# Kernel tuning notes

Hardware: AMD Instinct MI355X
Metric: run time of the kernel (lower is better)

The kernel has to match this reference:

```python
import jax, jax.numpy as jnp
import numpy as np

B, S, T = 2048, 32, 32
D, H = 128, 256       # cle_dim, rnn_dim
VS, VT = 256, 256     # source/target char vocab
BOW = 1               # MorphoDataset.Factor.BOW


def setup_inputs() -> dict:
    key = jax.random.key(0)
    ks = jax.random.split(key, 16)
    n = lambda k, sh: (jax.random.normal(k, sh, jnp.float32) * 0.05)
    inp = {
        "src_emb": n(ks[0], (VS, D)),
        "tgt_emb": n(ks[1], (VT, D)),
        "enc_f_W": n(ks[2], (D, 3 * H)),
        "enc_f_U": n(ks[3], (H, 3 * H)),
        "enc_f_b": jnp.zeros((2, 3 * H), jnp.float32),
        "enc_b_W": n(ks[4], (D, 3 * H)),
        "enc_b_U": n(ks[5], (H, 3 * H)),
        "enc_b_b": jnp.zeros((2, 3 * H), jnp.float32),
        "dec_W": n(ks[6], (D + H, 3 * H)),
        "dec_U": n(ks[7], (H, 3 * H)),
        "dec_b": jnp.zeros((2, 3 * H), jnp.float32),
        "out_W": n(ks[8], (H, VT)),
        "out_b": jnp.zeros((VT,), jnp.float32),
        "att_src_W": n(ks[9], (H, H)),
        "att_src_b": jnp.zeros((H,), jnp.float32),
        "att_st_W": n(ks[10], (H, H)),
        "att_st_b": jnp.zeros((H,), jnp.float32),
        "att_v": n(ks[11], (H, 1)),
        "att_v_b": jnp.zeros((1,), jnp.float32),
        "source_ids": jax.random.randint(ks[12], (B, S), 0, VS, jnp.int32),
        "target_ids": jax.random.randint(ks[13], (B, T), 0, VT, jnp.int32),
    }
    return inp


def _gru_step(h, x, W, U, b):
    # Keras GRU, reset_after=True: separate input/recurrent biases b[0], b[1]
    gx = x @ W + b[0]
    gh = h @ U + b[1]
    xz, xr, xh = jnp.split(gx, 3, axis=-1)
    hz, hr, hh = jnp.split(gh, 3, axis=-1)
    z = jax.nn.sigmoid(xz + hz)
    r = jax.nn.sigmoid(xr + hr)
    c = jnp.tanh(xh + r * hh)
    return z * h + (1.0 - z) * c


def _gru_scan(x_tbd, W, U, b):
    # x_tbd: [S, B, D] -> outputs [S, B, H]
    h0 = jnp.zeros((x_tbd.shape[1], U.shape[0]), x_tbd.dtype)
    def step(h, x):
        h = _gru_step(h, x, W, U, b)
        return h, h
    _, ys = jax.lax.scan(step, h0, x_tbd)
    return ys


def reference(src_emb, tgt_emb, enc_f_W, enc_f_U, enc_f_b, enc_b_W, enc_b_U, enc_b_b,
              dec_W, dec_U, dec_b, out_W, out_b, att_src_W, att_src_b,
              att_st_W, att_st_b, att_v, att_v_b, source_ids, target_ids):
    # ---- Encoder: bidirectional GRU, merge_mode='sum' ----
    x = src_emb[source_ids]                      # [B, S, D]
    x_t = jnp.transpose(x, (1, 0, 2))            # [S, B, D]
    fwd = _gru_scan(x_t, enc_f_W, enc_f_U, enc_f_b)
    bwd = _gru_scan(x_t[::-1], enc_b_W, enc_b_U, enc_b_b)[::-1]
    source_states = jnp.transpose(fwd + bwd, (1, 0, 2))  # [B, S, H]

    # projected source states are constant across decoder steps -> precompute
    proj_src = source_states @ att_src_W + att_src_b     # [B, S, H]

    def attend(inp, h):
        p = h @ att_st_W + att_st_b                      # [B, H]
        e = jnp.tanh(proj_src + p[:, None, :]) @ att_v + att_v_b  # [B, S, 1]
        w = jax.nn.softmax(e, axis=1)                    # softmax over source positions
        ctx = jnp.sum(source_states * w, axis=1)         # [B, H]
        return jnp.concatenate([inp, ctx], axis=1)       # [B, D+H]

    # ---- Decoder (teacher forcing) ----
    h0 = source_states[:, 0]                             # [B, H]
    bow = jnp.broadcast_to(tgt_emb[BOW], (source_ids.shape[0], tgt_emb.shape[1]))
    inp0 = attend(bow, h0)

    def dstep(carry, tgt_t):
        h, inp = carry
        h = _gru_step(h, inp, dec_W, dec_U, dec_b)       # GRUCell step
        logits = h @ out_W + out_b                       # [B, VT]
        nxt = attend(tgt_emb[tgt_t], h)
        return (h, nxt), logits

    _, logits = jax.lax.scan(dstep, (h0, inp0), jnp.transpose(target_ids))
    return jnp.transpose(logits, (1, 0, 2))              # [B, T, VT]
```

## Files before the change

kernel.cpp:

```cpp
#include <hip/hip_runtime.h>
#include <math.h>

#define B_  2048
#define S_  32
#define T_  32
#define D_  128
#define H_  256
#define G3  768
#define VT_ 256
#define BOW_ 1

typedef __attribute__((ext_vector_type(8))) short short8;
typedef __attribute__((ext_vector_type(4))) float f32x4;
typedef __attribute__((ext_vector_type(8))) unsigned short us8;
typedef unsigned short u16;

__device__ inline u16 f2bf(float x) {
  union { float f; unsigned u; } v; v.f = x;
  unsigned r = v.u + 0x7FFFu + ((v.u >> 16) & 1u);
  return (u16)(r >> 16);
}
__device__ inline float bf2f(u16 b) {
  union { unsigned u; float f; } v; v.u = ((unsigned)b) << 16; return v.f;
}
__device__ inline int swz(int r) { return ((r ^ (r >> 3)) & 7) << 3; }
__device__ inline float sigm(float x) { return 1.f / (1.f + expf(-x)); }

struct TMat { const float* src; u16* dhi; u16* dlo; int R; int C; int tile0; };
struct TPack { TMat m[10]; };

__global__ __launch_bounds__(256)
void wsplit_t(TPack P) {
  int bx = blockIdx.x;
  TMat M = P.m[0];
  #pragma unroll
  for (int i = 1; i < 10; i++) if (bx >= P.m[i].tile0) M = P.m[i];
  int ti = bx - M.tile0;
  int tilesR = M.R >> 6;
  int rt = ti % tilesR, ct = ti / tilesR;
  int r0 = rt * 64, c0 = ct * 64;
  __shared__ float ts[64][65];
  int tid = threadIdx.x;
  int cx = tid & 63, ry = tid >> 6;
  #pragma unroll
  for (int i = 0; i < 16; i++) {
    int r = ry * 16 + i;
    ts[r][cx] = M.src[(size_t)(r0 + r) * M.C + c0 + cx];
  }
  __syncthreads();
  int rx = tid & 63, cy = tid >> 6;
  #pragma unroll
  for (int i = 0; i < 16; i++) {
    int cc = cy * 16 + i;
    float v = ts[rx][cc];
    u16 hi = f2bf(v);
    size_t o = (size_t)(c0 + cc) * M.R + r0 + rx;
    M.dhi[o] = hi;
    M.dlo[o] = f2bf(v - bf2f(hi));
  }
}

__global__ __launch_bounds__(256)
void esplit(const float* a, const float* b, u16* ah, u16* al, u16* bh, u16* bl, int n) {
  int i = blockIdx.x * 256 + threadIdx.x;
  if (i >= 2 * n) return;
  const float* s = (i < n) ? a : b;
  u16* dh = (i < n) ? ah : bh;
  u16* dl = (i < n) ? al : bl;
  int j = (i < n) ? i : i - n;
  float v = s[j];
  u16 hi = f2bf(v);
  dh[j] = hi; dl[j] = f2bf(v - bf2f(hi));
}

struct PLeg {
  const u16* Ahi; const u16* Alo; int lda;
  const u16* Bthi; const u16* Btlo; int ldb;
  const float* bias; void* C; int ldc; int cmode;
  int M, N, K;
};

__global__ __launch_bounds__(256)
void gemm_pl(PLeg l0, PLeg l1) {
  PLeg L = blockIdx.z ? l1 : l0;
  int n0 = blockIdx.x * 128; if (n0 >= L.N) return;
  int m0 = blockIdx.y * 128; if (m0 >= L.M) return;
  __shared__ u16 As[128 * 64];
  __shared__ u16 Bs[128 * 64];
  int tid = threadIdx.x;
  int lane = tid & 63, wv = tid >> 6;
  int wr = (wv >> 1) * 64, wc = (wv & 1) * 64;
  int fr = lane & 15, fk = (lane >> 4) * 8;
  f32x4 acc[4][4];
  #pragma unroll
  for (int m = 0; m < 4; m++)
    #pragma unroll
    for (int n = 0; n < 4; n++) acc[m][n] = (f32x4){0.f, 0.f, 0.f, 0.f};

  int s_row = tid >> 1, s_part = tid & 1;

  for (int k0 = 0; k0 < L.K; k0 += 32) {
    if (k0) __syncthreads();
    int swA = swz(s_row);
    {
      const u16* src = (s_part ? L.Alo : L.Ahi) + (size_t)(m0 + s_row) * L.lda + k0;
      #pragma unroll
      for (int q = 0; q < 4; q++)
        *(us8*)&As[(s_row * 64 + s_part * 32 + q * 8) ^ swA] = *(const us8*)(src + q * 8);
    }
    {
      const u16* src = (s_part ? L.Btlo : L.Bthi) + (size_t)(n0 + s_row) * L.ldb + k0;
      #pragma unroll
      for (int q = 0; q < 4; q++)
        *(us8*)&Bs[(s_row * 64 + s_part * 32 + q * 8) ^ swA] = *(const us8*)(src + q * 8);
    }
    __syncthreads();
    short8 bhi[4], blo[4];
    #pragma unroll
    for (int n = 0; n < 4; n++) {
      int cc = wc + n * 16 + fr; int sw = swz(cc);
      bhi[n] = *(const short8*)&Bs[(cc * 64 + fk) ^ sw];
      blo[n] = *(const short8*)&Bs[(cc * 64 + 32 + fk) ^ sw];
    }
    #pragma unroll
    for (int m = 0; m < 4; m++) {
      int r = wr + m * 16 + fr; int sw = swz(r);
      short8 ahi = *(const short8*)&As[(r * 64 + fk) ^ sw];
      short8 alo = *(const short8*)&As[(r * 64 + 32 + fk) ^ sw];
      #pragma unroll
      for (int n = 0; n < 4; n++) {
        acc[m][n] = __builtin_amdgcn_mfma_f32_16x16x32_bf16(ahi, bhi[n], acc[m][n], 0, 0, 0);
        acc[m][n] = __builtin_amdgcn_mfma_f32_16x16x32_bf16(ahi, blo[n], acc[m][n], 0, 0, 0);
        acc[m][n] = __builtin_amdgcn_mfma_f32_16x16x32_bf16(alo, bhi[n], acc[m][n], 0, 0, 0);
      }
    }
  }
  int rbase = (lane >> 4) * 4;
  #pragma unroll
  for (int m = 0; m < 4; m++)
    #pragma unroll
    for (int rr = 0; rr < 4; rr++) {
      int row = m0 + wr + m * 16 + rbase + rr;
      #pragma unroll
      for (int n = 0; n < 4; n++) {
        int col = n0 + wc + n * 16 + fr;
        float v = acc[m][n][rr];
        if (L.bias) v += L.bias[col];
        if (L.cmode == 0)      ((float*)L.C)[(size_t)row * L.ldc + col] = v;
        else if (L.cmode == 1) ((u16*)L.C)[(size_t)row * L.ldc + col] = f2bf(v);
        else {
          size_t o = (((size_t)(row & (B_ - 1))) * T_ + (row >> 11)) * VT_ + col;
          ((float*)L.C)[o] = v;
        }
      }
    }
}

struct GruDesc {
  const u16 *a0H, *a0L;
  const u16 *a1H, *a1L;
  const u16 *b0H, *b0L;
  const u16 *b1H, *b1L;
  const float *gxT;
  const float *bias0, *bias1;
  const float *hold;
  const u16 *holdH, *holdL;
  float *hnew;
  u16 *hh, *hl;
  u16 *ssH, *ssL;
  const int *ids;
  int ssmode;
  int sidx, rev;
};

template<int MODE>
__global__ __launch_bounds__(256)
void gru_step(GruDesc d0, GruDesc d1) {
  GruDesc D = blockIdx.z ? d1 : d0;
  constexpr int KT  = MODE ? 512 : 256;
  constexpr int KT8 = KT / 8;
  constexpr int MF  = MODE ? 1 : 2;
  constexpr int NST = KT / 32;
  __shared__ __align__(16) u16 As[2 * 32 * KT];

  int m0 = blockIdx.y * 32;
  int tid = threadIdx.x;
  int lane = tid & 63, wv = tid >> 6;
  int fr = lane & 15, kq = lane >> 4;
  int jn, rb0;
  if (MODE == 0) { jn = blockIdx.x * 64 + wv * 16 + fr; rb0 = 0; }
  else           { jn = blockIdx.x * 32 + (wv & 1) * 16 + fr; rb0 = (wv >> 1) * 16; }

  constexpr int PER_T = (2 * 32 * KT8) / 256;
  #pragma unroll
  for (int i = 0; i < PER_T; i++) {
    int s = tid + i * 256;
    int p = s / (32 * KT8);
    int rem = s - p * (32 * KT8);
    int row = rem / KT8;
    int kb = rem - row * KT8;
    int k = kb * 8;
    const u16* src;
    if (MODE == 0) {
      src = (p ? D.a0L : D.a0H) + (size_t)(m0 + row) * 256 + k;
    } else {
      src = (k < 256) ? (p ? D.a0L : D.a0H) + (size_t)(m0 + row) * 256 + k
                      : (p ? D.a1L : D.a1H) + (size_t)(m0 + row) * 256 + (k - 256);
    }
    *(us8*)&As[(s ^ (row & 7)) * 8] = *(const us8*)src;
  }
  __syncthreads();

  f32x4 acc[4][MF];
  #pragma unroll
  for (int a = 0; a < 4; a++)
    #pragma unroll
    for (int mf = 0; mf < MF; mf++) acc[a][mf] = (f32x4){0.f, 0.f, 0.f, 0.f};

  #pragma unroll
  for (int i = 0; i < NST; i++) {
    const u16 *BH, *BL; int bk, ai2;
    if (MODE == 0)    { BH = D.b0H; BL = D.b0L; bk = i * 32; ai2 = 2; }
    else if (i < 8)   { BH = D.b0H; BL = D.b0L; bk = i * 32; ai2 = 2; }
    else              { BH = D.b1H; BL = D.b1L; bk = (i - 8) * 32; ai2 = 3; }
    short8 ah[MF], al[MF];
    #pragma unroll
    for (int mf = 0; mf < MF; mf++) {
      int rp = rb0 + mf * 16 + fr;
      int kb = i * 4 + kq;
      ah[mf] = *(const short8*)&As[((rp * KT8 + kb) ^ (fr & 7)) * 8];
      al[mf] = *(const short8*)&As[((32 * KT8 + rp * KT8 + kb) ^ (fr & 7)) * 8];
    }
    #pragma unroll
    for (int st = 0; st < 3; st++) {
      size_t ro = (size_t)(st * 256 + jn) * 256 + bk + kq * 8;
      short8 bh = *(const short8*)(BH + ro);
      short8 bl = *(const short8*)(BL + ro);
      int ai = (st < 2) ? st : ai2;
      #pragma unroll
      for (int mf = 0; mf < MF; mf++) {
        acc[ai][mf] = __builtin_amdgcn_mfma_f32_16x16x32_bf16(ah[mf], bh, acc[ai][mf], 0, 0, 0);
        acc[ai][mf] = __builtin_amdgcn_mfma_f32_16x16x32_bf16(ah[mf], bl, acc[ai][mf], 0, 0, 0);
        acc[ai][mf] = __builtin_amdgcn_mfma_f32_16x16x32_bf16(al[mf], bh, acc[ai][mf], 0, 0, 0);
      }
    }
  }

  int rbase = kq * 4;
  int j = jn;
  float b0z = D.bias0[j],       b1z = D.bias1[j];
  float b0r = D.bias0[256 + j], b1r = D.bias1[256 + j];
  float b0c = D.bias0[512 + j], b1c = D.bias1[512 + j];
  #pragma unroll
  for (int mf = 0; mf < MF; mf++)
    #pragma unroll
    for (int rr = 0; rr < 4; rr++) {
      int b = m0 + rb0 + mf * 16 + rbase + rr;
      size_t o = (size_t)b * H_ + j;
      int id;
      if (MODE == 0) id = D.ids[b * S_ + (D.rev ? (S_ - 1 - D.sidx) : D.sidx)];
      else           id = (D.sidx == 0) ? BOW_ : D.ids[b * T_ + D.sidx - 1];
      const float* T = D.gxT + (size_t)id * G3;
      float z = sigm(acc[0][mf][rr] + T[j] + b0z + b1z);
      float r = sigm(acc[1][mf][rr] + T[256 + j] + b0r + b1r);
      float xc = T[512 + j] + b0c + (MODE ? acc[3][mf][rr] : 0.f);
      float c = tanhf(xc + r * (acc[2][mf][rr] + b1c));
      float hprev = D.hold ? D.hold[o] : (bf2f(D.holdH[o]) + bf2f(D.holdL[o]));
      float hn = z * hprev + (1.f - z) * c;
      D.hnew[o] = hn;
      u16 hi = f2bf(hn);
      D.hh[o] = hi; D.hl[o] = f2bf(hn - bf2f(hi));
      if (MODE == 0) {
        if (D.ssmode == 1) {
          D.ssH[o] = hi; D.ssL[o] = f2bf(hn - bf2f(hi));
        } else if (D.ssmode == 2) {
          float v = bf2f(D.ssH[o]) + bf2f(D.ssL[o]) + hn;
          u16 vh = f2bf(v);
          D.ssH[o] = vh; D.ssL[o] = f2bf(v - bf2f(vh));
        }
      }
    }
}

__global__ __launch_bounds__(256)
void attend_k(const u16* __restrict__ projbf, const u16* __restrict__ ssH,
              const float* __restrict__ p, const float* __restrict__ att_v,
              u16* __restrict__ ctxh, u16* __restrict__ ctxl) {
  int b = blockIdx.x;
  int tid = threadIdx.x;
  int lane = tid & 63;
  int wv = tid >> 6;
  __shared__ float e_s[S_];
  __shared__ float w_s[S_];
  float pq[4], vq[4];
  #pragma unroll
  for (int q = 0; q < 4; q++) {
    pq[q] = p[(size_t)b * H_ + q * 64 + lane];
    vq[q] = att_v[q * 64 + lane];
  }
  float pv[8][4];
  #pragma unroll
  for (int i = 0; i < 8; i++) {
    const u16* pr = projbf + ((size_t)(wv * 8 + i) * B_ + b) * H_;
    #pragma unroll
    for (int q = 0; q < 4; q++) pv[i][q] = bf2f(pr[q * 64 + lane]);
  }
  u16 sv[S_];
  #pragma unroll
  for (int s = 0; s < S_; s++) sv[s] = ssH[((size_t)s * B_ + b) * H_ + tid];

  #pragma unroll
  for (int i = 0; i < 8; i++) {
    float part = 0.f;
    #pragma unroll
    for (int q = 0; q < 4; q++)
      part += tanhf(pv[i][q] + pq[q]) * vq[q];
    #pragma unroll
    for (int off = 32; off; off >>= 1)
      part += __shfl_xor(part, off);
    if (lane == 0) e_s[wv * 8 + i] = part;
  }
  __syncthreads();
  float m = -1e30f;
  #pragma unroll
  for (int s = 0; s < S_; s++) m = fmaxf(m, e_s[s]);
  float den = 0.f;
  #pragma unroll
  for (int s = 0; s < S_; s++) den += expf(e_s[s] - m);
  if (tid < S_) w_s[tid] = expf(e_s[tid] - m) / den;
  __syncthreads();
  float acc = 0.f;
  #pragma unroll
  for (int s = 0; s < S_; s++)
    acc = fmaf(w_s[s], bf2f(sv[s]), acc);
  u16 hi = f2bf(acc);
  size_t o = (size_t)b * H_ + tid;
  ctxh[o] = hi; ctxl[o] = f2bf(acc - bf2f(hi));
}

extern "C" void kernel_launch(void* const* d_in, const int* in_sizes, int n_in,
                              void* d_out, int out_size, void* d_ws, size_t ws_size,
                              hipStream_t stream) {
  const float* src_emb   = (const float*)d_in[0];
  const float* tgt_emb   = (const float*)d_in[1];
  const float* enc_f_W   = (const float*)d_in[2];
  const float* enc_f_U   = (const float*)d_in[3];
  const float* enc_f_b   = (const float*)d_in[4];
  const float* enc_b_W   = (const float*)d_in[5];
  const float* enc_b_U   = (const float*)d_in[6];
  const float* enc_b_b   = (const float*)d_in[7];
  const float* dec_W     = (const float*)d_in[8];
  const float* dec_U     = (const float*)d_in[9];
  const float* dec_b     = (const float*)d_in[10];
  const float* out_W     = (const float*)d_in[11];
  const float* out_b     = (const float*)d_in[12];
  const float* att_src_W = (const float*)d_in[13];
  const float* att_src_b = (const float*)d_in[14];
  const float* att_st_W  = (const float*)d_in[15];
  const float* att_st_b  = (const float*)d_in[16];
  const float* att_v     = (const float*)d_in[17];
  const int* source_ids  = (const int*)d_in[19];
  const int* target_ids  = (const int*)d_in[20];
  float* out = (float*)d_out;

  char* base = (char*)d_ws;
  size_t off = 0;
  auto allocB = [&](size_t bytes) { void* p = base + off; off = (off + bytes + 255) & ~255UL; return p; };
  const size_t BH = (size_t)B_ * H_;

  u16* ssH    = (u16*)allocB((size_t)S_ * BH * 2);
  u16* ssL    = (u16*)allocB((size_t)S_ * BH * 2);
  u16* projbf = (u16*)allocB((size_t)S_ * BH * 2);
  float* pbuf = (float*)allocB(BH * 4);
  u16* ctxh = (u16*)allocB(BH * 2);
  u16* ctxl = (u16*)allocB(BH * 2);

  float* encF0 = (float*)allocB(2 * BH * 4);
  u16*  encPl0 = (u16*)allocB(4 * BH * 2);
  float* encF1 = (float*)allocB(2 * BH * 4);
  u16*  encPl1 = (u16*)allocB(4 * BH * 2);
  float* encF[2][2]  = { { encF0, encF0 + BH }, { encF1, encF1 + BH } };
  u16*  encH[2][2]   = { { encPl0, encPl0 + 2 * BH }, { encPl1, encPl1 + 2 * BH } };
  u16*  encL[2][2]   = { { encPl0 + BH, encPl0 + 3 * BH }, { encPl1 + BH, encPl1 + 3 * BH } };

  float* hDecF[2] = { (float*)allocB(BH * 4), (float*)allocB(BH * 4) };
  u16* hAllH = (u16*)allocB((size_t)T_ * BH * 2);
  u16* hAllL = (u16*)allocB((size_t)T_ * BH * 2);

  auto planes2 = [&](size_t n, u16*& h, u16*& l) { h = (u16*)allocB(n * 2); l = (u16*)allocB(n * 2); };
  u16 *UtFh,*UtFl,*UtBh,*UtBl,*WtFh,*WtFl,*WtBh,*WtBl;
  u16 *dUth,*dUtl,*dWcth,*dWctl,*dWxth,*dWxtl;
  u16 *oWth,*oWtl,*aStth,*aSttl,*aSrth,*aSrtl;
  u16 *sEh,*sEl,*tEh,*tEl;
  planes2((size_t)G3*H_, UtFh, UtFl);   planes2((size_t)G3*H_, UtBh, UtBl);
  planes2((size_t)G3*D_, WtFh, WtFl);   planes2((size_t)G3*D_, WtBh, WtBl);
  planes2((size_t)G3*H_, dUth, dUtl);   planes2((size_t)G3*H_, dWcth, dWctl);
  planes2((size_t)G3*D_, dWxth, dWxtl);
  planes2((size_t)H_*VT_, oWth, oWtl);
  planes2((size_t)H_*H_, aSrth, aSrtl);
  planes2((size_t)H_*H_, aStth, aSttl);
  planes2((size_t)VT_*D_, sEh, sEl);    planes2((size_t)VT_*D_, tEh, tEl);
  float* Tf = (float*)allocB((size_t)VT_ * G3 * 4);
  float* Tb = (float*)allocB((size_t)VT_ * G3 * 4);
  float* Td = (float*)allocB((size_t)VT_ * G3 * 4);

  TPack P;
  P.m[0] = { enc_f_U,          UtFh, UtFl, 256, 768, 0   };
  P.m[1] = { enc_b_U,          UtBh, UtBl, 256, 768, 48  };
  P.m[2] = { dec_U,            dUth, dUtl, 256, 768, 96  };
  P.m[3] = { dec_W + 128 * G3, dWcth, dWctl, 256, 768, 144 };
  P.m[4] = { enc_f_W,          WtFh, WtFl, 128, 768, 192 };
  P.m[5] = { enc_b_W,          WtBh, WtBl, 128, 768, 216 };
  P.m[6] = { dec_W,            dWxth, dWxtl, 128, 768, 240 };
  P.m[7] = { out_W,            oWth, oWtl, 256, 256, 264 };
  P.m[8] = { att_src_W,        aSrth, aSrtl, 256, 256, 280 };
  P.m[9] = { att_st_W,         aStth, aSttl, 256, 256, 296 };
  wsplit_t<<<312, 256, 0, stream>>>(P);
  esplit<<<(2 * VT_ * D_ + 255) / 256, 256, 0, stream>>>(src_emb, tgt_emb, sEh, sEl, tEh, tEl, VT_ * D_);

  {
    PLeg tf = { sEh, sEl, D_, WtFh, WtFl, D_, nullptr, Tf, G3, 0, VT_, G3, D_ };
    PLeg tb = { sEh, sEl, D_, WtBh, WtBl, D_, nullptr, Tb, G3, 0, VT_, G3, D_ };
    gemm_pl<<<dim3(6, 2, 2), 256, 0, stream>>>(tf, tb);
    PLeg td = { tEh, tEl, D_, dWxth, dWxtl, D_, nullptr, Td, G3, 0, VT_, G3, D_ };
    gemm_pl<<<dim3(6, 2, 1), 256, 0, stream>>>(td, td);
  }

  hipMemsetAsync(encF0, 0, 2 * BH * 4, stream);
  hipMemsetAsync(encPl0, 0, 4 * BH * 2, stream);

  for (int s = 0; s < S_; s++) {
    int p = s & 1;
    GruDesc dd[2];
    for (int d = 0; d < 2; d++) {
      GruDesc& D = dd[d];
      D.a0H = encH[p][d]; D.a0L = encL[p][d];
      D.a1H = nullptr; D.a1L = nullptr;
      D.b0H = d ? UtBh : UtFh; D.b0L = d ? UtBl : UtFl;
      D.b1H = nullptr; D.b1L = nullptr;
      D.gxT = d ? Tb : Tf;
      D.bias0 = d ? enc_b_b : enc_f_b;
      D.bias1 = (d ? enc_b_b : enc_f_b) + G3;
      D.hold = encF[p][d]; D.holdH = nullptr; D.holdL = nullptr;
      D.hnew = encF[p ^ 1][d];
      D.hh = encH[p ^ 1][d]; D.hl = encL[p ^ 1][d];
      int pos = d ? (S_ - 1 - s) : s;
      D.ssH = ssH + (size_t)pos * BH; D.ssL = ssL + (size_t)pos * BH;
      D.ids = source_ids;
      D.ssmode = (s < S_ / 2) ? 1 : 2;
      D.sidx = s; D.rev = d;
    }
    gru_step<0><<<dim3(4, 64, 2), 256, 0, stream>>>(dd[0], dd[1]);
  }

  {
    PLeg proj = { ssH, ssL, H_, aSrth, aSrtl, H_, att_src_b, projbf, H_, 1, S_ * B_, H_, H_ };
    PLeg p0   = { ssH, ssL, H_, aStth, aSttl, H_, att_st_b,  pbuf,   H_, 0, B_,      H_, H_ };
    gemm_pl<<<dim3(2, 512, 2), 256, 0, stream>>>(proj, p0);
  }
  attend_k<<<B_, 256, 0, stream>>>(projbf, ssH, pbuf, att_v, ctxh, ctxl);

  for (int t = 0; t < T_; t++) {
    int p = t & 1;
    GruDesc D = {};
    D.a0H = t ? hAllH + (size_t)(t - 1) * BH : ssH;
    D.a0L = t ? hAllL + (size_t)(t - 1) * BH : ssL;
    D.a1H = ctxh; D.a1L = ctxl;
    D.b0H = dUth;  D.b0L = dUtl;
    D.b1H = dWcth; D.b1L = dWctl;
    D.gxT = Td;
    D.bias0 = dec_b; D.bias1 = dec_b + G3;
    if (t == 0) { D.hold = nullptr; D.holdH = ssH; D.holdL = ssL; }
    else        { D.hold = hDecF[p]; D.holdH = nullptr; D.holdL = nullptr; }
    D.hnew = hDecF[p ^ 1];
    D.hh = hAllH + (size_t)t * BH; D.hl = hAllL + (size_t)t * BH;
    D.ssH = nullptr; D.ssL = nullptr;
    D.ids = target_ids;
    D.ssmode = 0; D.sidx = t; D.rev = 0;
    gru_step<1><<<dim3(8, 64, 1), 256, 0, stream>>>(D, D);

    if (t < T_ - 1) {
      PLeg LP = { hAllH + (size_t)t * BH, hAllL + (size_t)t * BH, H_,
                  aStth, aSttl, H_, att_st_b, pbuf, H_, 0, B_, H_, H_ };
      gemm_pl<<<dim3(2, 16, 1), 256, 0, stream>>>(LP, LP);
      attend_k<<<B_, 256, 0, stream>>>(projbf, ssH, pbuf, att_v, ctxh, ctxl);
    }
  }

  {
    PLeg LO = { hAllH, hAllL, H_, oWth, oWtl, H_, out_b, out, 0, 2, T_ * B_, VT_, H_ };
    gemm_pl<<<dim3(2, 512, 1), 256, 0, stream>>>(LO, LO);
  }
}
```

Baseline: 3.604 ms.

## Fuse encoder and decoder time loops into persistent cooperative kernels

Replaces the per-timestep encoder GRU launches and the per-step decoder GRU, projection-GEMM and attention launches with two persistent cooperative kernels that use grid-wide syncs between steps. The decoder attention phase fuses the query projection GEMM with the score, softmax and context computation in 128 blocks. The goal is to remove roughly 120 kernel launches and their launch gaps. In exchange it depends on cooperative-launch support and enough occupancy for 512 co-resident blocks, leaves most blocks idle during the attention phase, and falls back to per-step launches otherwise.

```diff
diff --git a/kernel.cpp b/kernel.cpp
--- a/kernel.cpp
+++ b/kernel.cpp
@@ -1,5 +1,8 @@
 #include <hip/hip_runtime.h>
+#include <hip/hip_cooperative_groups.h>
 #include <math.h>
+
+namespace cg = cooperative_groups;
 
 #define B_  2048
 #define S_  32
@@ -156,132 +159,6 @@
     }
 }
 
-struct GruDesc {
-  const u16 *a0H, *a0L;
-  const u16 *a1H, *a1L;
-  const u16 *b0H, *b0L;
-  const u16 *b1H, *b1L;
-  const float *gxT;
-  const float *bias0, *bias1;
-  const float *hold;
-  const u16 *holdH, *holdL;
-  float *hnew;
-  u16 *hh, *hl;
-  u16 *ssH, *ssL;
-  const int *ids;
-  int ssmode;
-  int sidx, rev;
-};
-
-template<int MODE>
-__global__ __launch_bounds__(256)
-void gru_step(GruDesc d0, GruDesc d1) {
-  GruDesc D = blockIdx.z ? d1 : d0;
-  constexpr int KT  = MODE ? 512 : 256;
-  constexpr int KT8 = KT / 8;
-  constexpr int MF  = MODE ? 1 : 2;
-  constexpr int NST = KT / 32;
-  __shared__ __align__(16) u16 As[2 * 32 * KT];
-
-  int m0 = blockIdx.y * 32;
-  int tid = threadIdx.x;
-  int lane = tid & 63, wv = tid >> 6;
-  int fr = lane & 15, kq = lane >> 4;
-  int jn, rb0;
-  if (MODE == 0) { jn = blockIdx.x * 64 + wv * 16 + fr; rb0 = 0; }
-  else           { jn = blockIdx.x * 32 + (wv & 1) * 16 + fr; rb0 = (wv >> 1) * 16; }
-
-  constexpr int PER_T = (2 * 32 * KT8) / 256;
-  #pragma unroll
-  for (int i = 0; i < PER_T; i++) {
-    int s = tid + i * 256;
-    int p = s / (32 * KT8);
-    int rem = s - p * (32 * KT8);
-    int row = rem / KT8;
-    int kb = rem - row * KT8;
-    int k = kb * 8;
-    const u16* src;
-    if (MODE == 0) {
-      src = (p ? D.a0L : D.a0H) + (size_t)(m0 + row) * 256 + k;
-    } else {
-      src = (k < 256) ? (p ? D.a0L : D.a0H) + (size_t)(m0 + row) * 256 + k
-                      : (p ? D.a1L : D.a1H) + (size_t)(m0 + row) * 256 + (k - 256);
-    }
-    *(us8*)&As[(s ^ (row & 7)) * 8] = *(const us8*)src;
-  }
-  __syncthreads();
-
-  f32x4 acc[4][MF];
-  #pragma unroll
-  for (int a = 0; a < 4; a++)
-    #pragma unroll
-    for (int mf = 0; mf < MF; mf++) acc[a][mf] = (f32x4){0.f, 0.f, 0.f, 0.f};
-
-  #pragma unroll
-  for (int i = 0; i < NST; i++) {
-    const u16 *BH, *BL; int bk, ai2;
-    if (MODE == 0)    { BH = D.b0H; BL = D.b0L; bk = i * 32; ai2 = 2; }
-    else if (i < 8)   { BH = D.b0H; BL = D.b0L; bk = i * 32; ai2 = 2; }
-    else              { BH = D.b1H; BL = D.b1L; bk = (i - 8) * 32; ai2 = 3; }
-    short8 ah[MF], al[MF];
-    #pragma unroll
-    for (int mf = 0; mf < MF; mf++) {
-      int rp = rb0 + mf * 16 + fr;
-      int kb = i * 4 + kq;
-      ah[mf] = *(const short8*)&As[((rp * KT8 + kb) ^ (fr & 7)) * 8];
-      al[mf] = *(const short8*)&As[((32 * KT8 + rp * KT8 + kb) ^ (fr & 7)) * 8];
-    }
-    #pragma unroll
-    for (int st = 0; st < 3; st++) {
-      size_t ro = (size_t)(st * 256 + jn) * 256 + bk + kq * 8;
-      short8 bh = *(const short8*)(BH + ro);
-      short8 bl = *(const short8*)(BL + ro);
-      int ai = (st < 2) ? st : ai2;
-      #pragma unroll
-      for (int mf = 0; mf < MF; mf++) {
-        acc[ai][mf] = __builtin_amdgcn_mfma_f32_16x16x32_bf16(ah[mf], bh, acc[ai][mf], 0, 0, 0);
-        acc[ai][mf] = __builtin_amdgcn_mfma_f32_16x16x32_bf16(ah[mf], bl, acc[ai][mf], 0, 0, 0);
-        acc[ai][mf] = __builtin_amdgcn_mfma_f32_16x16x32_bf16(al[mf], bh, acc[ai][mf], 0, 0, 0);
-      }
-    }
-  }
-
-  int rbase = kq * 4;
-  int j = jn;
-  float b0z = D.bias0[j],       b1z = D.bias1[j];
-  float b0r = D.bias0[256 + j], b1r = D.bias1[256 + j];
-  float b0c = D.bias0[512 + j], b1c = D.bias1[512 + j];
-  #pragma unroll
-  for (int mf = 0; mf < MF; mf++)
-    #pragma unroll
-    for (int rr = 0; rr < 4; rr++) {
-      int b = m0 + rb0 + mf * 16 + rbase + rr;
-      size_t o = (size_t)b * H_ + j;
-      int id;
-      if (MODE == 0) id = D.ids[b * S_ + (D.rev ? (S_ - 1 - D.sidx) : D.sidx)];
-      else           id = (D.sidx == 0) ? BOW_ : D.ids[b * T_ + D.sidx - 1];
-      const float* T = D.gxT + (size_t)id * G3;
-      float z = sigm(acc[0][mf][rr] + T[j] + b0z + b1z);
-      float r = sigm(acc[1][mf][rr] + T[256 + j] + b0r + b1r);
-      float xc = T[512 + j] + b0c + (MODE ? acc[3][mf][rr] : 0.f);
-      float c = tanhf(xc + r * (acc[2][mf][rr] + b1c));
-      float hprev = D.hold ? D.hold[o] : (bf2f(D.holdH[o]) + bf2f(D.holdL[o]));
-      float hn = z * hprev + (1.f - z) * c;
-      D.hnew[o] = hn;
-      u16 hi = f2bf(hn);
-      D.hh[o] = hi; D.hl[o] = f2bf(hn - bf2f(hi));
-      if (MODE == 0) {
-        if (D.ssmode == 1) {
-          D.ssH[o] = hi; D.ssL[o] = f2bf(hn - bf2f(hi));
-        } else if (D.ssmode == 2) {
-          float v = bf2f(D.ssH[o]) + bf2f(D.ssL[o]) + hn;
-          u16 vh = f2bf(v);
-          D.ssH[o] = vh; D.ssL[o] = f2bf(v - bf2f(vh));
-        }
-      }
-    }
-}
-
 __global__ __launch_bounds__(256)
 void attend_k(const u16* __restrict__ projbf, const u16* __restrict__ ssH,
               const float* __restrict__ p, const float* __restrict__ att_v,
@@ -336,6 +213,368 @@
   u16 hi = f2bf(acc);
   size_t o = (size_t)b * H_ + tid;
   ctxh[o] = hi; ctxl[o] = f2bf(acc - bf2f(hi));
+}
+
+struct EncP {
+  u16* hH[2][2]; u16* hL[2][2];
+  float* hF[2][2];
+  const u16 *bUH[2], *bUL[2];
+  const float *gxT[2];
+  const float *bias[2];
+  u16 *ssH, *ssL;
+  const int *ids;
+};
+
+__device__ __forceinline__ void enc_step_body(const EncP& P, int s, u16* As) {
+  int bid = blockIdx.x;
+  int d = bid >> 8, rem = bid & 255;
+  int x = rem & 3, y = rem >> 2;
+  int m0 = y * 32;
+  int tid = threadIdx.x;
+  int lane = tid & 63, wv = tid >> 6;
+  int fr = lane & 15, kq = lane >> 4;
+  int jn = x * 64 + wv * 16 + fr;
+  const size_t BHsz = (size_t)B_ * H_;
+
+  const u16 *bUH = P.bUH[d], *bUL = P.bUL[d];
+  const float *bias0 = P.bias[d], *bias1 = P.bias[d] + G3;
+  int par = s & 1;
+  const u16 *a0H = P.hH[par][d], *a0L = P.hL[par][d];
+
+  #pragma unroll
+  for (int i = 0; i < 8; i++) {
+    int sl = tid + i * 256;
+    int pl = sl >> 10;
+    int rm = sl & 1023;
+    int row = rm >> 5;
+    const u16* src = (pl ? a0L : a0H) + (size_t)(m0 + row) * 256 + (rm & 31) * 8;
+    *(us8*)&As[(sl ^ (row & 7)) * 8] = *(const us8*)src;
+  }
+  __syncthreads();
+
+  f32x4 acc[3][2];
+  #pragma unroll
+  for (int a = 0; a < 3; a++)
+    #pragma unroll
+    for (int mf = 0; mf < 2; mf++) acc[a][mf] = (f32x4){0.f, 0.f, 0.f, 0.f};
+
+  #pragma unroll
+  for (int i = 0; i < 8; i++) {
+    short8 ah[2], al[2];
+    #pragma unroll
+    for (int mf = 0; mf < 2; mf++) {
+      int rp = mf * 16 + fr;
+      int kb = i * 4 + kq;
+      ah[mf] = *(const short8*)&As[((rp * 32 + kb) ^ (fr & 7)) * 8];
+      al[mf] = *(const short8*)&As[((1024 + rp * 32 + kb) ^ (fr & 7)) * 8];
+    }
+    #pragma unroll
+    for (int st = 0; st < 3; st++) {
+      size_t ro = (size_t)(st * 256 + jn) * 256 + i * 32 + kq * 8;
+      short8 bh = *(const short8*)(bUH + ro);
+      short8 bl = *(const short8*)(bUL + ro);
+      #pragma unroll
+      for (int mf = 0; mf < 2; mf++) {
+        acc[st][mf] = __builtin_amdgcn_mfma_f32_16x16x32_bf16(ah[mf], bh, acc[st][mf], 0, 0, 0);
+        acc[st][mf] = __builtin_amdgcn_mfma_f32_16x16x32_bf16(ah[mf], bl, acc[st][mf], 0, 0, 0);
+        acc[st][mf] = __builtin_amdgcn_mfma_f32_16x16x32_bf16(al[mf], bh, acc[st][mf], 0, 0, 0);
+      }
+    }
+  }
+
+  float b0z = bias0[jn] + bias1[jn];
+  float b0r = bias0[256 + jn] + bias1[256 + jn];
+  float bxc = bias0[512 + jn];
+  float bhc = bias1[512 + jn];
+  const float *gxT = P.gxT[d];
+  int rbase = kq * 4;
+  float* hoF = P.hF[par][d];
+  float* hnF = P.hF[par ^ 1][d];
+  u16* hnH = P.hH[par ^ 1][d];
+  u16* hnL = P.hL[par ^ 1][d];
+  int pos = d ? (S_ - 1 - s) : s;
+  u16* ssHp = P.ssH + (size_t)pos * BHsz;
+  u16* ssLp = P.ssL + (size_t)pos * BHsz;
+  int ssmode = (s < S_ / 2) ? 1 : 2;
+  #pragma unroll
+  for (int mf = 0; mf < 2; mf++)
+    #pragma unroll
+    for (int rr = 0; rr < 4; rr++) {
+      int b = m0 + mf * 16 + rbase + rr;
+      size_t o = (size_t)b * H_ + jn;
+      int id = P.ids[b * S_ + (d ? (S_ - 1 - s) : s)];
+      const float* T = gxT + (size_t)id * G3;
+      float z = sigm(acc[0][mf][rr] + T[jn] + b0z);
+      float r = sigm(acc[1][mf][rr] + T[256 + jn] + b0r);
+      float c = tanhf(T[512 + jn] + bxc + r * (acc[2][mf][rr] + bhc));
+      float hn = z * hoF[o] + (1.f - z) * c;
+      hnF[o] = hn;
+      u16 hi = f2bf(hn);
+      u16 lo = f2bf(hn - bf2f(hi));
+      hnH[o] = hi; hnL[o] = lo;
+      if (ssmode == 1) {
+        ssHp[o] = hi; ssLp[o] = lo;
+      } else {
+        float v = bf2f(ssHp[o]) + bf2f(ssLp[o]) + hn;
+        u16 vh = f2bf(v);
+        ssHp[o] = vh; ssLp[o] = f2bf(v - bf2f(vh));
+      }
+    }
+}
+
+template<int COOP>
+__global__ __launch_bounds__(256, 2)
+void enc_all(EncP P, int s_single) {
+  __shared__ __align__(16) u16 As[2 * 32 * 256];
+  if constexpr (COOP) {
+    cg::grid_group grid = cg::this_grid();
+    for (int s = 0; s < S_; s++) {
+      enc_step_body(P, s, As);
+      if (s < S_ - 1) grid.sync();
+    }
+  } else {
+    enc_step_body(P, s_single, As);
+  }
+}
+
+struct DecP {
+  u16 *hAH, *hAL;
+  const u16 *s0H, *s0L;
+  float *hF[2];
+  u16 *ctxH, *ctxL;
+  const u16 *bUH, *bUL, *bCH, *bCL;
+  const float *gxT;
+  const float *bias;
+  const u16 *sWH, *sWL;
+  const float *stb;
+  const u16 *projbf, *ssHall;
+  const float *attv;
+  const int *ids;
+};
+
+__device__ __forceinline__ void dec_g_body(const DecP& P, int t, u16* As) {
+  int bid = blockIdx.x;
+  int tid = threadIdx.x;
+  int lane = tid & 63, wv = tid >> 6;
+  int fr = lane & 15, kq = lane >> 4;
+  int xg = bid & 7, yg = bid >> 3;
+  int m0 = yg * 32;
+  int jn = xg * 32 + (wv & 1) * 16 + fr;
+  int rb0 = (wv >> 1) * 16;
+  const size_t BHsz = (size_t)B_ * H_;
+  int par = t & 1;
+  const u16 *a0H = t ? P.hAH + (size_t)(t - 1) * BHsz : P.s0H;
+  const u16 *a0L = t ? P.hAL + (size_t)(t - 1) * BHsz : P.s0L;
+
+  f32x4 acc[4];
+  #pragma unroll
+  for (int a = 0; a < 4; a++) acc[a] = (f32x4){0.f, 0.f, 0.f, 0.f};
+
+  #pragma unroll
+  for (int i = 0; i < 8; i++) {
+    int sl = tid + i * 256;
+    int pl = sl >> 10;
+    int rm = sl & 1023;
+    int row = rm >> 5;
+    const u16* src = (pl ? a0L : a0H) + (size_t)(m0 + row) * 256 + (rm & 31) * 8;
+    *(us8*)&As[(sl ^ (row & 7)) * 8] = *(const us8*)src;
+  }
+  __syncthreads();
+  #pragma unroll
+  for (int i = 0; i < 8; i++) {
+    int rp = rb0 + fr;
+    int kb = i * 4 + kq;
+    short8 ah = *(const short8*)&As[((rp * 32 + kb) ^ (fr & 7)) * 8];
+    short8 al = *(const short8*)&As[((1024 + rp * 32 + kb) ^ (fr & 7)) * 8];
+    #pragma unroll
+    for (int st = 0; st < 3; st++) {
+      size_t ro = (size_t)(st * 256 + jn) * 256 + i * 32 + kq * 8;
+      short8 bh = *(const short8*)(P.bUH + ro);
+      short8 bl = *(const short8*)(P.bUL + ro);
+      int ai = (st < 2) ? st : 2;
+      acc[ai] = __builtin_amdgcn_mfma_f32_16x16x32_bf16(ah, bh, acc[ai], 0, 0, 0);
+      acc[ai] = __builtin_amdgcn_mfma_f32_16x16x32_bf16(ah, bl, acc[ai], 0, 0, 0);
+      acc[ai] = __builtin_amdgcn_mfma_f32_16x16x32_bf16(al, bh, acc[ai], 0, 0, 0);
+    }
+  }
+  __syncthreads();
+  #pragma unroll
+  for (int i = 0; i < 8; i++) {
+    int sl = tid + i * 256;
+    int pl = sl >> 10;
+    int rm = sl & 1023;
+    int row = rm >> 5;
+    const u16* src = (pl ? P.ctxL : P.ctxH) + (size_t)(m0 + row) * 256 + (rm & 31) * 8;
+    *(us8*)&As[(sl ^ (row & 7)) * 8] = *(const us8*)src;
+  }
+  __syncthreads();
+  #pragma unroll
+  for (int i = 0; i < 8; i++) {
+    int rp = rb0 + fr;
+    int kb = i * 4 + kq;
+    short8 ah = *(const short8*)&As[((rp * 32 + kb) ^ (fr & 7)) * 8];
+    short8 al = *(const short8*)&As[((1024 + rp * 32 + kb) ^ (fr & 7)) * 8];
+    #pragma unroll
+    for (int st = 0; st < 3; st++) {
+      size_t ro = (size_t)(st * 256 + jn) * 256 + i * 32 + kq * 8;
+      short8 bh = *(const short8*)(P.bCH + ro);
+      short8 bl = *(const short8*)(P.bCL + ro);
+      int ai = (st < 2) ? st : 3;
+      acc[ai] = __builtin_amdgcn_mfma_f32_16x16x32_bf16(ah, bh, acc[ai], 0, 0, 0);
+      acc[ai] = __builtin_amdgcn_mfma_f32_16x16x32_bf16(ah, bl, acc[ai], 0, 0, 0);
+      acc[ai] = __builtin_amdgcn_mfma_f32_16x16x32_bf16(al, bh, acc[ai], 0, 0, 0);
+    }
+  }
+
+  float b0z = P.bias[jn] + P.bias[G3 + jn];
+  float b0r = P.bias[256 + jn] + P.bias[G3 + 256 + jn];
+  float bxc = P.bias[512 + jn];
+  float bhc = P.bias[G3 + 512 + jn];
+  int rbase = kq * 4;
+  float* hoF = P.hF[par];
+  float* hnF = P.hF[par ^ 1];
+  u16* hnH = P.hAH + (size_t)t * BHsz;
+  u16* hnL = P.hAL + (size_t)t * BHsz;
+  #pragma unroll
+  for (int rr = 0; rr < 4; rr++) {
+    int b = m0 + rb0 + rbase + rr;
+    size_t o = (size_t)b * H_ + jn;
+    int id = (t == 0) ? BOW_ : P.ids[b * T_ + t - 1];
+    const float* T = P.gxT + (size_t)id * G3;
+    float z = sigm(acc[0][rr] + T[jn] + b0z);
+    float r = sigm(acc[1][rr] + T[256 + jn] + b0r);
+    float c = tanhf(T[512 + jn] + bxc + acc[3][rr] + r * (acc[2][rr] + bhc));
+    float hprev = t ? hoF[o] : (bf2f(P.s0H[o]) + bf2f(P.s0L[o]));
+    float hn = z * hprev + (1.f - z) * c;
+    hnF[o] = hn;
+    u16 hi = f2bf(hn);
+    hnH[o] = hi; hnL[o] = f2bf(hn - bf2f(hi));
+  }
+}
+
+__device__ __forceinline__ void dec_la_body(const DecP& P, int t, u16* As) {
+  int bid = blockIdx.x;
+  if (bid >= 128) return;
+  int tid = threadIdx.x;
+  int lane = tid & 63, wv = tid >> 6;
+  int fr = lane & 15, kq = lane >> 4;
+  const size_t BHsz = (size_t)B_ * H_;
+  u16* hstage = As;
+  float* p_lds = (float*)(As + 8192);
+  float* e_lds = (float*)As;
+  int r0 = bid * 16;
+  float vq[4];
+  #pragma unroll
+  for (int q = 0; q < 4; q++) vq[q] = P.attv[q * 64 + lane];
+
+  const u16* hH_ = P.hAH + (size_t)t * BHsz;
+  const u16* hL_ = P.hAL + (size_t)t * BHsz;
+  #pragma unroll
+  for (int i = 0; i < 4; i++) {
+    int sl = tid + i * 256;
+    int pl = sl >> 9;
+    int rm = sl & 511;
+    int row = rm >> 5;
+    int k = (rm & 31) * 8;
+    const u16* src = (pl ? hL_ : hH_) + (size_t)(r0 + row) * 256 + k;
+    *(us8*)&hstage[(sl ^ (row & 7)) * 8] = *(const us8*)src;
+  }
+  __syncthreads();
+  f32x4 pacc[4];
+  #pragma unroll
+  for (int n = 0; n < 4; n++) pacc[n] = (f32x4){0.f, 0.f, 0.f, 0.f};
+  #pragma unroll
+  for (int c = 0; c < 8; c++) {
+    int kb = c * 4 + kq;
+    short8 ah = *(const short8*)&hstage[((fr * 32 + kb) ^ (fr & 7)) * 8];
+    short8 al = *(const short8*)&hstage[((512 + fr * 32 + kb) ^ (fr & 7)) * 8];
+    #pragma unroll
+    for (int n = 0; n < 4; n++) {
+      int j = wv * 64 + n * 16 + fr;
+      size_t ro = (size_t)j * 256 + c * 32 + kq * 8;
+      short8 bh = *(const short8*)(P.sWH + ro);
+      short8 bl = *(const short8*)(P.sWL + ro);
+      pacc[n] = __builtin_amdgcn_mfma_f32_16x16x32_bf16(ah, bh, pacc[n], 0, 0, 0);
+      pacc[n] = __builtin_amdgcn_mfma_f32_16x16x32_bf16(ah, bl, pacc[n], 0, 0, 0);
+      pacc[n] = __builtin_amdgcn_mfma_f32_16x16x32_bf16(al, bh, pacc[n], 0, 0, 0);
+    }
+  }
+  __syncthreads();
+  #pragma unroll
+  for (int n = 0; n < 4; n++) {
+    int j = wv * 64 + n * 16 + fr;
+    float bj = P.stb[j];
+    #pragma unroll
+    for (int rr = 0; rr < 4; rr++)
+      p_lds[(kq * 4 + rr) * 256 + j] = pacc[n][rr] + bj;
+  }
+  __syncthreads();
+  #pragma unroll
+  for (int u = 0; u < 4; u++) {
+    int lr = wv * 4 + u;
+    int b = r0 + lr;
+    float pq[4];
+    #pragma unroll
+    for (int q = 0; q < 4; q++) pq[q] = p_lds[lr * 256 + q * 64 + lane];
+    #pragma unroll 8
+    for (int s2 = 0; s2 < S_; s2++) {
+      const u16* pr = P.projbf + ((size_t)s2 * B_ + b) * H_;
+      float part = 0.f;
+      #pragma unroll
+      for (int q = 0; q < 4; q++)
+        part += tanhf(bf2f(pr[q * 64 + lane]) + pq[q]) * vq[q];
+      #pragma unroll
+      for (int off = 32; off; off >>= 1) part += __shfl_xor(part, off);
+      if (lane == 0) e_lds[lr * 32 + s2] = part;
+    }
+  }
+  __syncthreads();
+  #pragma unroll
+  for (int u = 0; u < 4; u++) {
+    int lr = wv * 4 + u;
+    int b = r0 + lr;
+    float m = -1e30f;
+    #pragma unroll
+    for (int s2 = 0; s2 < S_; s2++) m = fmaxf(m, e_lds[lr * 32 + s2]);
+    float wsr[S_]; float den = 0.f;
+    #pragma unroll
+    for (int s2 = 0; s2 < S_; s2++) { wsr[s2] = expf(e_lds[lr * 32 + s2] - m); den += wsr[s2]; }
+    float inv = 1.f / den;
+    float cacc[4] = {0.f, 0.f, 0.f, 0.f};
+    #pragma unroll 8
+    for (int s2 = 0; s2 < S_; s2++) {
+      float w = wsr[s2] * inv;
+      #pragma unroll
+      for (int q = 0; q < 4; q++)
+        cacc[q] = fmaf(w, bf2f(P.ssHall[((size_t)s2 * B_ + b) * H_ + q * 64 + lane]), cacc[q]);
+    }
+    #pragma unroll
+    for (int q = 0; q < 4; q++) {
+      float v = cacc[q];
+      u16 hi = f2bf(v);
+      size_t o = (size_t)b * H_ + q * 64 + lane;
+      P.ctxH[o] = hi; P.ctxL[o] = f2bf(v - bf2f(hi));
+    }
+  }
+}
+
+template<int COOP>
+__global__ __launch_bounds__(256, 2)
+void dec_all(DecP P, int t_single, int phase) {
+  __shared__ __align__(16) u16 As[2 * 32 * 256];
+  if constexpr (COOP) {
+    cg::grid_group grid = cg::this_grid();
+    for (int t = 0; t < T_; t++) {
+      dec_g_body(P, t, As);
+      if (t == T_ - 1) break;
+      grid.sync();
+      dec_la_body(P, t, As);
+      grid.sync();
+    }
+  } else {
+    if (phase == 0) dec_g_body(P, t_single, As);
+    else            dec_la_body(P, t_single, As);
+  }
 }
 
 extern "C" void kernel_launch(void* const* d_in, const int* in_sizes, int n_in,
@@ -429,28 +668,40 @@
   hipMemsetAsync(encF0, 0, 2 * BH * 4, stream);
   hipMemsetAsync(encPl0, 0, 4 * BH * 2, stream);
 
-  for (int s = 0; s < S_; s++) {
-    int p = s & 1;
-    GruDesc dd[2];
+  int devId = 0;
+  hipGetDevice(&devId);
+  int coopAttr = 0;
+  hipDeviceGetAttribute(&coopAttr, hipDeviceAttributeCooperativeLaunch, devId);
+  int numCU = 0;
+  hipDeviceGetAttribute(&numCU, hipDeviceAttributeMultiprocessorCount, devId);
+  int nbE = 0, nbD = 0;
+  hipOccupancyMaxActiveBlocksPerMultiprocessor(&nbE, (const void*)enc_all<1>, 256, 0);
+  hipOccupancyMaxActiveBlocksPerMultiprocessor(&nbD, (const void*)dec_all<1>, 256, 0);
+  bool coopE = coopAttr && ((long)nbE * numCU >= 512);
+  bool coopD = coopAttr && ((long)nbD * numCU >= 512);
+
+  EncP Pe;
+  for (int par = 0; par < 2; par++)
     for (int d = 0; d < 2; d++) {
-      GruDesc& D = dd[d];
-      D.a0H = encH[p][d]; D.a0L = encL[p][d];
-      D.a1H = nullptr; D.a1L = nullptr;
-      D.b0H = d ? UtBh : UtFh; D.b0L = d ? UtBl : UtFl;
-      D.b1H = nullptr; D.b1L = nullptr;
-      D.gxT = d ? Tb : Tf;
-      D.bias0 = d ? enc_b_b : enc_f_b;
-      D.bias1 = (d ? enc_b_b : enc_f_b) + G3;
-      D.hold = encF[p][d]; D.holdH = nullptr; D.holdL = nullptr;
-      D.hnew = encF[p ^ 1][d];
-      D.hh = encH[p ^ 1][d]; D.hl = encL[p ^ 1][d];
-      int pos = d ? (S_ - 1 - s) : s;
-      D.ssH = ssH + (size_t)pos * BH; D.ssL = ssL + (size_t)pos * BH;
-      D.ids = source_ids;
-      D.ssmode = (s < S_ / 2) ? 1 : 2;
-      D.sidx = s; D.rev = d;
-    }
-    gru_step<0><<<dim3(4, 64, 2), 256, 0, stream>>>(dd[0], dd[1]);
+      Pe.hH[par][d] = encH[par][d];
+      Pe.hL[par][d] = encL[par][d];
+      Pe.hF[par][d] = encF[par][d];
+    }
+  Pe.bUH[0] = UtFh; Pe.bUL[0] = UtFl;
+  Pe.bUH[1] = UtBh; Pe.bUL[1] = UtBl;
+  Pe.gxT[0] = Tf;   Pe.gxT[1] = Tb;
+  Pe.bias[0] = enc_f_b; Pe.bias[1] = enc_b_b;
+  Pe.ssH = ssH; Pe.ssL = ssL;
+  Pe.ids = source_ids;
+  if (coopE) {
+    int zero = 0;
+    void* eargs[] = { &Pe, &zero };
+    hipError_t e = hipLaunchCooperativeKernel((void*)enc_all<1>, dim3(512), dim3(256), eargs, 0, stream);
+    if (e != hipSuccess) { (void)hipGetLastError(); coopE = false; }
+  }
+  if (!coopE) {
+    for (int s = 0; s < S_; s++)
+      enc_all<0><<<dim3(512), 256, 0, stream>>>(Pe, s);
   }
 
   {
@@ -460,30 +711,30 @@
   }
   attend_k<<<B_, 256, 0, stream>>>(projbf, ssH, pbuf, att_v, ctxh, ctxl);
 
-  for (int t = 0; t < T_; t++) {
-    int p = t & 1;
-    GruDesc D = {};
-    D.a0H = t ? hAllH + (size_t)(t - 1) * BH : ssH;
-    D.a0L = t ? hAllL + (size_t)(t - 1) * BH : ssL;
-    D.a1H = ctxh; D.a1L = ctxl;
-    D.b0H = dUth;  D.b0L = dUtl;
-    D.b1H = dWcth; D.b1L = dWctl;
-    D.gxT = Td;
-    D.bias0 = dec_b; D.bias1 = dec_b + G3;
-    if (t == 0) { D.hold = nullptr; D.holdH = ssH; D.holdL = ssL; }
-    else        { D.hold = hDecF[p]; D.holdH = nullptr; D.holdL = nullptr; }
-    D.hnew = hDecF[p ^ 1];
-    D.hh = hAllH + (size_t)t * BH; D.hl = hAllL + (size_t)t * BH;
-    D.ssH = nullptr; D.ssL = nullptr;
-    D.ids = target_ids;
-    D.ssmode = 0; D.sidx = t; D.rev = 0;
-    gru_step<1><<<dim3(8, 64, 1), 256, 0, stream>>>(D, D);
-
-    if (t < T_ - 1) {
-      PLeg LP = { hAllH + (size_t)t * BH, hAllL + (size_t)t * BH, H_,
-                  aStth, aSttl, H_, att_st_b, pbuf, H_, 0, B_, H_, H_ };
-      gemm_pl<<<dim3(2, 16, 1), 256, 0, stream>>>(LP, LP);
-      attend_k<<<B_, 256, 0, stream>>>(projbf, ssH, pbuf, att_v, ctxh, ctxl);
+  DecP Pd;
+  Pd.hAH = hAllH; Pd.hAL = hAllL;
+  Pd.s0H = ssH;   Pd.s0L = ssL;
+  Pd.hF[0] = hDecF[0]; Pd.hF[1] = hDecF[1];
+  Pd.ctxH = ctxh; Pd.ctxL = ctxl;
+  Pd.bUH = dUth; Pd.bUL = dUtl; Pd.bCH = dWcth; Pd.bCL = dWctl;
+  Pd.gxT = Td;
+  Pd.bias = dec_b;
+  Pd.sWH = aStth; Pd.sWL = aSttl;
+  Pd.stb = att_st_b;
+  Pd.projbf = projbf; Pd.ssHall = ssH;
+  Pd.attv = att_v;
+  Pd.ids = target_ids;
+  if (coopD) {
+    int zero = 0, zero2 = 0;
+    void* dargs[] = { &Pd, &zero, &zero2 };
+    hipError_t e = hipLaunchCooperativeKernel((void*)dec_all<1>, dim3(512), dim3(256), dargs, 0, stream);
+    if (e != hipSuccess) { (void)hipGetLastError(); coopD = false; }
+  }
+  if (!coopD) {
+    for (int t = 0; t < T_; t++) {
+      dec_all<0><<<dim3(512), 256, 0, stream>>>(Pd, t, 0);
+      if (t < T_ - 1)
+        dec_all<0><<<dim3(128), 256, 0, stream>>>(Pd, t, 1);
     }
   }
 
```

After: 8.503 ms. +136.0%, slower.
